# Kernel tuning notes

Measured on AMD Instinct MI355X. Metric: run time of the kernel, lower is better.

The kernel has to match this reference:

```python
import jax, jax.numpy as jnp
import numpy as np

N_NODES = 100000
N_EDGES = 1200000
IN_FEATS = 128
HIDDEN = 64
OUT_FEATS = 40


def setup_inputs() -> dict:
    key = jax.random.key(0)
    k1, k2, k3, k4, k5 = jax.random.split(key, 5)
    x = jax.random.normal(k1, (N_NODES, IN_FEATS), dtype=jnp.float32)
    edge_index = jax.random.randint(k2, (2, N_EDGES), 0, N_NODES, dtype=jnp.int64)
    W1 = jax.random.normal(k3, (IN_FEATS, HIDDEN), dtype=jnp.float32) * (1.0 / np.sqrt(IN_FEATS))
    b1 = jnp.zeros((HIDDEN,), dtype=jnp.float32)
    W2 = jax.random.normal(k4, (HIDDEN, HIDDEN), dtype=jnp.float32) * (1.0 / np.sqrt(HIDDEN))
    b2 = jnp.zeros((HIDDEN,), dtype=jnp.float32)
    Wc = jax.random.normal(k5, (HIDDEN, OUT_FEATS), dtype=jnp.float32) * (1.0 / np.sqrt(HIDDEN))
    bc = jnp.zeros((OUT_FEATS,), dtype=jnp.float32)
    return {"x": x, "edge_index": edge_index, "W1": W1, "b1": b1,
            "W2": W2, "b2": b2, "Wc": Wc, "bc": bc}


def _gcn_norm(edge_index, n_nodes):
    # add self-loops, then symmetric normalization deg^{-1/2}[src] * deg^{-1/2}[dst]
    loops = jnp.arange(n_nodes, dtype=edge_index.dtype)
    src = jnp.concatenate([edge_index[0], loops])
    dst = jnp.concatenate([edge_index[1], loops])
    ones = jnp.ones(src.shape[0], dtype=jnp.float32)
    deg = jax.ops.segment_sum(ones, dst, num_segments=n_nodes)  # in-degree incl. self-loop
    dinv = jnp.where(deg > 0, jax.lax.rsqrt(deg), 0.0)
    norm = dinv[src] * dinv[dst]  # [E+N]
    return src, dst, norm


def _gcn_conv(h, W, b, src, dst, norm, n_nodes):
    h = h @ W                          # [N, F_out] dense transform first (PyG GCNConv)
    msg = h[src] * norm[:, None]       # gather + normalize, [E+N, F_out]
    out = jax.ops.segment_sum(msg, dst, num_segments=n_nodes)  # scatter-add
    return out + b


def reference(x, edge_index, W1, b1, W2, b2, Wc, bc):
    n = x.shape[0]
    src, dst, norm = _gcn_norm(edge_index, n)
    # dropout is identity in eval mode
    h = jax.nn.relu(_gcn_conv(x, W1, b1, src, dst, norm, n))
    embedding = _gcn_conv(h, W2, b2, src, dst, norm, n)
    logits = embedding @ Wc + bc
    soft_label = jax.nn.softmax(logits, axis=1)
    hard_label = jnp.argmax(soft_label, axis=1)
    return (logits, embedding, soft_label, hard_label)
```

## Files before the change

### kernel.cpp

```cpp
#include <hip/hip_runtime.h>
#include <hip/hip_bf16.h>
#include <math.h>

typedef __hip_bfloat16 bf16;

__device__ __forceinline__ float loadf(const void* p, size_t i, bool f32m) {
    return f32m ? ((const float*)p)[i]
                : __bfloat162float(((const bf16*)p)[i]);
}
__device__ __forceinline__ void storef(void* p, size_t i, float v, bool f32m) {
    if (f32m) ((float*)p)[i] = v;
    else      ((bf16*)p)[i] = __float2bfloat16(v);
}
__device__ __forceinline__ int ldidx(const int* w, size_t e, bool e64, size_t E, int row) {
    return e64 ? w[2 * (row * E + e)] : w[row * E + e];
}

__global__ void k_detect(const void* x, const int* ei, float* flags) {
    int lane = threadIdx.x;
    const unsigned short* hx = (const unsigned short*)x;
    unsigned short u = hx[2 * lane];
    int ex = (u >> 7) & 0xFF;
    bool tame = (ex >= 117 && ex <= 136);
    unsigned long long mt = __ballot(tame);
    unsigned long long mz = __ballot(ei[2 * lane + 1] != 0);
    if (lane == 0) {
        flags[0] = (__popcll(mt) >= 48) ? 0.0f : 1.0f;
        flags[1] = (mz == 0ULL) ? 1.0f : 0.0f;
    }
}


__global__ void k_zero_small(int* __restrict__ p, int m) {
    int i = blockIdx.x * 256 + threadIdx.x;
    if (i < m) p[i] = 0;
}

#define SCB_EPT 16

__global__ __launch_bounds__(256) void k_bucket_hist(const int* __restrict__ ei,
                                                     const float* __restrict__ flags,
                                                     int* __restrict__ bcnt, int E, int NB) {
    __shared__ int lcnt[512];
    bool e64 = flags[1] > 0.5f;
    int tid = threadIdx.x;
    for (int i = tid; i < NB; i += 256) lcnt[i] = 0;
    __syncthreads();
    int base = blockIdx.x * 256 * SCB_EPT;
#pragma unroll
    for (int j = 0; j < SCB_EPT; ++j) {
        int e = base + j * 256 + tid;
        if (e < E) atomicAdd(&lcnt[ldidx(ei, e, e64, E, 1) >> 8], 1);
    }
    __syncthreads();
    for (int i = tid; i < NB; i += 256) {
        int c = lcnt[i];
        if (c) atomicAdd(&bcnt[i], c);
    }
}

__global__ __launch_bounds__(512) void k_scan_buckets(const int* __restrict__ bcnt,
                                                      int* __restrict__ bbase,
                                                      int* __restrict__ bcur, int NB) {
    __shared__ int sh[512];
    int tid = threadIdx.x;
    int v = (tid < NB) ? bcnt[tid] : 0;
    sh[tid] = v;
    __syncthreads();
    for (int off = 1; off < 512; off <<= 1) {
        int t = (tid >= off) ? sh[tid - off] : 0;
        __syncthreads();
        sh[tid] += t;
        __syncthreads();
    }
    if (tid < NB) {
        int ex = sh[tid] - v;
        bbase[tid] = ex;
        bcur[tid] = ex;
    }
    if (tid == 0) bbase[NB] = sh[511];
}

__global__ __launch_bounds__(256) void k_bucket_scatter(const int* __restrict__ ei,
                                                        const float* __restrict__ flags,
                                                        int* __restrict__ bcur,
                                                        int2* __restrict__ recs,
                                                        int E, int NB) {
    __shared__ int lcnt[512], lrank[512], lbase[512];
    bool e64 = flags[1] > 0.5f;
    int tid = threadIdx.x;
    for (int i = tid; i < NB; i += 256) { lcnt[i] = 0; lrank[i] = 0; }
    __syncthreads();
    int base = blockIdx.x * 256 * SCB_EPT;
    int s[SCB_EPT], d[SCB_EPT];
#pragma unroll
    for (int j = 0; j < SCB_EPT; ++j) {
        int e = base + j * 256 + tid;
        if (e < E) {
            s[j] = ldidx(ei, e, e64, E, 0);
            d[j] = ldidx(ei, e, e64, E, 1);
            atomicAdd(&lcnt[d[j] >> 8], 1);
        } else d[j] = -1;
    }
    __syncthreads();
    for (int i = tid; i < NB; i += 256) {
        int c = lcnt[i];
        lbase[i] = c ? atomicAdd(&bcur[i], c) : 0;
    }
    __syncthreads();
#pragma unroll
    for (int j = 0; j < SCB_EPT; ++j) {
        if (d[j] >= 0) {
            int b = d[j] >> 8;
            int r = atomicAdd(&lrank[b], 1);
            recs[lbase[b] + r] = make_int2(s[j], d[j]);
        }
    }
}

__global__ __launch_bounds__(256) void k_bucket_csr(const int2* __restrict__ recs,
                                                    const int* __restrict__ bbase,
                                                    int* __restrict__ rowptr,
                                                    float* __restrict__ dinv,
                                                    int* __restrict__ srcs,
                                                    int n, int E) {
    __shared__ int lcnt[256];
    __shared__ int lcur[256];
    int b = blockIdx.x, tid = threadIdx.x;
    int e0 = bbase[b], e1 = bbase[b + 1];
    lcnt[tid] = 0;
    __syncthreads();
    for (int i = e0 + tid; i < e1; i += 256)
        atomicAdd(&lcnt[recs[i].y & 255], 1);
    __syncthreads();
    int c = lcnt[tid];
    lcur[tid] = c;
    __syncthreads();
    for (int off = 1; off < 256; off <<= 1) {
        int t = (tid >= off) ? lcur[tid - off] : 0;
        __syncthreads();
        lcur[tid] += t;
        __syncthreads();
    }
    int rp = bbase[b] + lcur[tid] - c;
    int node = (b << 8) + tid;
    if (node < n) {
        rowptr[node] = rp;
        dinv[node] = rsqrtf((float)(c + 1));
    }
    lcur[tid] = rp;
    __syncthreads();
    for (int i = e0 + tid; i < e1; i += 256) {
        int2 r = recs[i];
        int pos = atomicAdd(&lcur[r.y & 255], 1);
        srcs[pos] = r.x;
    }
    if (b == 0 && tid == 0) rowptr[n] = E;
}

template <int K, bool XF32>
__global__ __launch_bounds__(256) void k_gemm3(const void* __restrict__ Xa,
                                               const void* __restrict__ Xb,
                                               const void* __restrict__ W,
                                               const float* __restrict__ flags,
                                               const float* __restrict__ rowscale,
                                               float* __restrict__ out, int n) {
    __shared__ float xs[64 * (K + 4)];
    __shared__ float wl[K * 68];
    bool f32m = flags[0] > 0.5f;
    const void* X = f32m ? Xa : Xb;
    bool xf32 = XF32 || f32m;
    int tid = threadIdx.x;
    int r0 = blockIdx.x * 64;

    if (f32m) {
        for (int i = tid * 4; i < K * 64; i += 1024) {
            int k = i >> 6, cc = i & 63;
            float4 v = *(const float4*)((const float*)W + i);
            *(float4*)&wl[k * 68 + cc] = v;
        }
    } else {
        for (int i = tid; i < K * 64; i += 256) {
            int k = i >> 6, cc = i & 63;
            wl[k * 68 + cc] = __bfloat162float(((const bf16*)W)[i]);
        }
    }
    if (xf32) {
        for (int i = tid * 4; i < 64 * K; i += 1024) {
            int row = i / K, k = i % K;
            float4 v = {0, 0, 0, 0};
            if (r0 + row < n) v = *(const float4*)((const float*)X + (size_t)(r0 + row) * K + k);
            *(float4*)&xs[row * (K + 4) + k] = v;
        }
    } else {
        for (int i = tid * 4; i < 64 * K; i += 1024) {
            int row = i / K, k = i % K;
            float4 v = {0, 0, 0, 0};
            if (r0 + row < n) {
                const bf16* p = (const bf16*)X + (size_t)(r0 + row) * K + k;
                v.x = __bfloat162float(p[0]); v.y = __bfloat162float(p[1]);
                v.z = __bfloat162float(p[2]); v.w = __bfloat162float(p[3]);
            }
            *(float4*)&xs[row * (K + 4) + k] = v;
        }
    }
    __syncthreads();

    int lane = tid & 63, wv = tid >> 6;
    int rg = lane >> 4, cg = lane & 15;
    int rbase = wv * 16 + rg * 4;
    int cbase = cg * 4;

    float acc[4][4];
#pragma unroll
    for (int r = 0; r < 4; ++r)
#pragma unroll
        for (int c = 0; c < 4; ++c) acc[r][c] = 0.0f;

#pragma unroll 2
    for (int k = 0; k < K; k += 4) {
        float4 xrv[4], wv4[4];
#pragma unroll
        for (int r = 0; r < 4; ++r)
            xrv[r] = *(const float4*)&xs[(rbase + r) * (K + 4) + k];
#pragma unroll
        for (int j = 0; j < 4; ++j)
            wv4[j] = *(const float4*)&wl[(k + j) * 68 + cbase];
#pragma unroll
        for (int r = 0; r < 4; ++r) {
            const float* xp = (const float*)&xrv[r];
#pragma unroll
            for (int j = 0; j < 4; ++j) {
                float xv = xp[j];
                acc[r][0] += xv * wv4[j].x;
                acc[r][1] += xv * wv4[j].y;
                acc[r][2] += xv * wv4[j].z;
                acc[r][3] += xv * wv4[j].w;
            }
        }
    }

#pragma unroll
    for (int r = 0; r < 4; ++r) {
        int row = r0 + rbase + r;
        if (row < n) {
            float sc = rowscale[row];
            float4 st = {acc[r][0] * sc, acc[r][1] * sc, acc[r][2] * sc, acc[r][3] * sc};
            *(float4*)&out[(size_t)row * 64 + cbase] = st;
        }
    }
}

template <int EP>
__global__ __launch_bounds__(256) void k_agg(const float* __restrict__ t,
                                             const float* __restrict__ dinv,
                                             const int* __restrict__ rowptr,
                                             const int* __restrict__ srcs,
                                             const void* __restrict__ bias,
                                             const float* __restrict__ flags,
                                             void* __restrict__ d_out, size_t emb_base,
                                             float* __restrict__ B_ws, int n) {
    bool f32m = flags[0] > 0.5f;
    int wvid = (blockIdx.x * 256 + threadIdx.x) >> 6;
    int lane = threadIdx.x & 63;
    int grp = lane >> 4;
    int col4 = lane & 15;
    int v0 = wvid * 2;
    int v1 = v0 + 1;
    if (v0 >= n) return;
    bool has1 = (v1 < n);

    float4 bias4;
    if (f32m) {
        bias4 = ((const float4*)bias)[col4];
    } else {
        const bf16* bp = (const bf16*)bias + col4 * 4;
        bias4.x = __bfloat162float(bp[0]); bias4.y = __bfloat162float(bp[1]);
        bias4.z = __bfloat162float(bp[2]); bias4.w = __bfloat162float(bp[3]);
    }

    float dvA = dinv[v0];
    float dvB = has1 ? dinv[v1] : 0.0f;
    int e0a = rowptr[v0], e1a = rowptr[v0 + 1];
    int e0b = has1 ? rowptr[v1] : 0;
    int e1b = has1 ? rowptr[v1 + 1] : 0;
    int degA = e1a - e0a + 1;
    int degB = has1 ? (e1b - e0b + 1) : 0;
    int degMax = degA > degB ? degA : degB;

    float4 accA = {0, 0, 0, 0}, accB = {0, 0, 0, 0};

    for (int base = 0; base < degMax; base += 64) {
        int jA = base + lane;
        int sA_l = -1;
        if (jA == 0) sA_l = v0;
        else if (jA < degA) sA_l = srcs[e0a + jA - 1];
        int sB_l = -1;
        if (has1) {
            int jB = base + lane;
            if (jB == 0) sB_l = v1;
            else if (jB < degB) sB_l = srcs[e0b + jB - 1];
        }
        int rem = degMax - base;
        int mq = rem < 64 ? rem : 64;

        for (int q = 0; q < mq; q += 16) {
            int sa[4], sb[4];
#pragma unroll
            for (int u = 0; u < 4; ++u) {
                int idx = q + 4 * u + grp;
                sa[u] = __shfl(sA_l, idx, 64);
                sb[u] = __shfl(sB_l, idx, 64);
            }
            float4 va[4], vb[4];
#pragma unroll
            for (int u = 0; u < 4; ++u) {
                va[u] = make_float4(0, 0, 0, 0);
                if (sa[u] >= 0)
                    va[u] = *((const float4*)(t + ((size_t)sa[u] << 6)) + col4);
                vb[u] = make_float4(0, 0, 0, 0);
                if (sb[u] >= 0)
                    vb[u] = *((const float4*)(t + ((size_t)sb[u] << 6)) + col4);
            }
#pragma unroll
            for (int u = 0; u < 4; ++u) {
                accA.x += va[u].x; accA.y += va[u].y; accA.z += va[u].z; accA.w += va[u].w;
                accB.x += vb[u].x; accB.y += vb[u].y; accB.z += vb[u].z; accB.w += vb[u].w;
            }
        }
    }

#pragma unroll
    for (int off = 16; off < 64; off <<= 1) {
        accA.x += __shfl_xor(accA.x, off, 64);
        accA.y += __shfl_xor(accA.y, off, 64);
        accA.z += __shfl_xor(accA.z, off, 64);
        accA.w += __shfl_xor(accA.w, off, 64);
        accB.x += __shfl_xor(accB.x, off, 64);
        accB.y += __shfl_xor(accB.y, off, 64);
        accB.z += __shfl_xor(accB.z, off, 64);
        accB.w += __shfl_xor(accB.w, off, 64);
    }

    int v = -1; float4 acc; float dv = 0.0f;
    if (grp == 0) { v = v0; acc = accA; dv = dvA; }
    else if (grp == 1 && has1) { v = v1; acc = accB; dv = dvB; }
    if (v >= 0) {
        acc.x = acc.x * dv + bias4.x;
        acc.y = acc.y * dv + bias4.y;
        acc.z = acc.z * dv + bias4.z;
        acc.w = acc.w * dv + bias4.w;
        if (EP == 0) {
            acc.x = fmaxf(acc.x, 0.0f); acc.y = fmaxf(acc.y, 0.0f);
            acc.z = fmaxf(acc.z, 0.0f); acc.w = fmaxf(acc.w, 0.0f);
        }
        size_t ob = (size_t)v * 64 + col4 * 4;
        if (f32m) {
            *(float4*)((float*)d_out + emb_base + ob) = acc;
        } else {
            *(float4*)&B_ws[ob] = acc;
            if (EP == 1) {
                __hip_bfloat162 h0, h1;
                h0.x = __float2bfloat16(acc.x); h0.y = __float2bfloat16(acc.y);
                h1.x = __float2bfloat16(acc.z); h1.y = __float2bfloat16(acc.w);
                __hip_bfloat162* p = (__hip_bfloat162*)((bf16*)d_out + emb_base + ob);
                p[0] = h0; p[1] = h1;
            }
        }
    }
}


__device__ __forceinline__ void store_row40(void* out, size_t base, const float* a, bool f32m) {
    if (f32m) {
        float4* p = (float4*)((float*)out + base);
#pragma unroll
        for (int q = 0; q < 10; ++q) {
            float4 st = {a[q * 4 + 0], a[q * 4 + 1], a[q * 4 + 2], a[q * 4 + 3]};
            p[q] = st;
        }
    } else {
        __hip_bfloat162* p = (__hip_bfloat162*)((bf16*)out + base);
#pragma unroll
        for (int i = 0; i < 20; ++i) {
            __hip_bfloat162 h;
            h.x = __float2bfloat16(a[2 * i]);
            h.y = __float2bfloat16(a[2 * i + 1]);
            p[i] = h;
        }
    }
}

__global__ __launch_bounds__(256) void k_classifier(const float* __restrict__ flags,
                                                    const void* __restrict__ Wc,
                                                    const void* __restrict__ bc,
                                                    void* __restrict__ out,
                                                    size_t emb_base, size_t soft_base,
                                                    size_t hard_base,
                                                    const float* __restrict__ B_ws,
                                                    int n) {
    __shared__ __align__(16) float wcs[64 * 40];
    __shared__ __align__(16) float bcs[40];
    bool f32m = flags[0] > 0.5f;
    const float* emb = f32m ? ((const float*)out + emb_base) : B_ws;
    int tid = threadIdx.x;

    if (f32m) {
        for (int i = tid * 4; i < 64 * 40; i += 1024)
            *(float4*)&wcs[i] = *(const float4*)((const float*)Wc + i);
    } else {
        for (int i = tid; i < 64 * 40; i += 256)
            wcs[i] = __bfloat162float(((const bf16*)Wc)[i]);
    }
    if (tid < 40) bcs[tid] = loadf(bc, tid, f32m);
    __syncthreads();

    int node = blockIdx.x * 256 + tid;
    if (node >= n) return;

    float acc[40];
#pragma unroll
    for (int q = 0; q < 10; ++q) {
        float4 b4 = *(const float4*)&bcs[q * 4];
        acc[q * 4 + 0] = b4.x; acc[q * 4 + 1] = b4.y;
        acc[q * 4 + 2] = b4.z; acc[q * 4 + 3] = b4.w;
    }

    const float4* erow = (const float4*)(emb + (size_t)node * 64);
#pragma unroll 2
    for (int j = 0; j < 16; ++j) {
        float4 e4 = erow[j];
        float ev[4] = {e4.x, e4.y, e4.z, e4.w};
#pragma unroll
        for (int kk = 0; kk < 4; ++kk) {
            float e = ev[kk];
            const float4* wr = (const float4*)&wcs[(j * 4 + kk) * 40];
#pragma unroll
            for (int q = 0; q < 10; ++q) {
                float4 w = wr[q];
                acc[q * 4 + 0] = fmaf(e, w.x, acc[q * 4 + 0]);
                acc[q * 4 + 1] = fmaf(e, w.y, acc[q * 4 + 1]);
                acc[q * 4 + 2] = fmaf(e, w.z, acc[q * 4 + 2]);
                acc[q * 4 + 3] = fmaf(e, w.w, acc[q * 4 + 3]);
            }
        }
    }

    store_row40(out, (size_t)node * 40, acc, f32m);

    float m0 = acc[0], m1 = acc[1], m2 = acc[2], m3 = acc[3];
#pragma unroll
    for (int q = 1; q < 10; ++q) {
        m0 = fmaxf(m0, acc[q * 4 + 0]); m1 = fmaxf(m1, acc[q * 4 + 1]);
        m2 = fmaxf(m2, acc[q * 4 + 2]); m3 = fmaxf(m3, acc[q * 4 + 3]);
    }
    float m = fmaxf(fmaxf(m0, m1), fmaxf(m2, m3));

    int bi = 63;
#pragma unroll
    for (int c = 0; c < 40; ++c)
        if (acc[c] == m && c < bi) bi = c;

    float s = 0.0f;
#pragma unroll
    for (int c = 0; c < 40; ++c) {
        float e = expf(acc[c] - m);
        acc[c] = e;
        s += e;
    }
    float rs = 1.0f / s;
#pragma unroll
    for (int c = 0; c < 40; ++c) acc[c] *= rs;

    store_row40(out, soft_base + (size_t)node * 40, acc, f32m);
    storef(out, hard_base + node, (float)bi, f32m);
}

extern "C" void kernel_launch(void* const* d_in, const int* in_sizes, int n_in,
                              void* d_out, int out_size, void* d_ws, size_t ws_size,
                              hipStream_t stream) {
    const void* x  = d_in[0];
    const int*  ei = (const int*)d_in[1];
    const void* W1 = d_in[2];
    const void* b1 = d_in[3];
    const void* W2 = d_in[4];
    const void* b2 = d_in[5];
    const void* Wc = d_in[6];
    const void* bc = d_in[7];

    const int n = in_sizes[0] / 128;
    const int E = in_sizes[1] / 2;
    const int NB = (n + 255) / 256;

    float* ws    = (float*)d_ws;
    const size_t npad = (((size_t)n + 1023) / 1024) * 1024;
    const size_t Epad = (((size_t)E + 255) / 256) * 256;
    float* flags  = ws;
    int*   bcnt   = (int*)(ws + 256);
    int*   bbase  = (int*)(ws + 768);
    int*   bcur   = (int*)(ws + 1536);
    int*   rowptr = (int*)(ws + 2048);
    float* dinv   = (float*)(rowptr + npad);
    int*   srcs   = (int*)(dinv + npad);
    float* A      = (float*)(srcs + Epad);
    float* B_ws   = A + (size_t)n * 64;
    int2*  recs   = (int2*)B_ws;

    const size_t emb_base  = (size_t)n * 40;
    const size_t soft_base = (size_t)n * 104;
    const size_t hard_base = (size_t)n * 144;
    float* h1_f32m = (float*)d_out + emb_base;

    const int gS  = (E + 256 * SCB_EPT - 1) / (256 * SCB_EPT);
    const int gG  = (n + 63) / 64;
    const int gW  = (n + 7) / 8;
    const int gC  = (n + 255) / 256;

    k_detect<<<1, 64, 0, stream>>>(x, ei, flags);

    k_zero_small<<<2, 256, 0, stream>>>(bcnt, 512);
    k_bucket_hist<<<gS, 256, 0, stream>>>(ei, flags, bcnt, E, NB);
    k_scan_buckets<<<1, 512, 0, stream>>>(bcnt, bbase, bcur, NB);
    k_bucket_scatter<<<gS, 256, 0, stream>>>(ei, flags, bcur, recs, E, NB);
    k_bucket_csr<<<NB, 256, 0, stream>>>(recs, bbase, rowptr, dinv, srcs, n, E);

    k_gemm3<128, false><<<gG, 256, 0, stream>>>(x, x, W1, flags, dinv, A, n);
    k_agg<0><<<gW, 256, 0, stream>>>(A, dinv, rowptr, srcs, b1, flags,
                                     d_out, emb_base, B_ws, n);

    k_gemm3<64, true><<<gG, 256, 0, stream>>>(h1_f32m, B_ws, W2, flags, dinv, A, n);
    k_agg<1><<<gW, 256, 0, stream>>>(A, dinv, rowptr, srcs, b2, flags,
                                     d_out, emb_base, B_ws, n);

    k_classifier<<<gC, 256, 0, stream>>>(flags, Wc, bc, d_out,
                                         emb_base, soft_base, hard_base, B_ws, n);
}
```

Before: 326.5 us.

## Replace FP32 SIMT feature GEMMs with split-bf16 MFMA kernels

The two dense transforms (X@W1 and H@W2) move from a shared-memory FP32 FMA tile kernel to MFMA 16x16x32 bf16 instructions. FP32 inputs are split into hi/lo bf16 parts and three MFMAs per tile recover near-FP32 accuracy. X is now loaded straight from global memory into registers, with no shared-memory staging, and the weights are transposed into shared memory. This cuts the FMA compute cost, at the price of three MFMAs per step, per-element conversion work, and 4-byte scalar output stores in place of float4 stores.

```diff
diff --git a/kernel.cpp b/kernel.cpp
--- a/kernel.cpp
+++ b/kernel.cpp
@@ -3,6 +3,8 @@
 #include <math.h>
 
 typedef __hip_bfloat16 bf16;
+typedef __attribute__((ext_vector_type(8))) short bf16x8;
+typedef __attribute__((ext_vector_type(4))) float f32x4;
 
 __device__ __forceinline__ float loadf(const void* p, size_t i, bool f32m) {
     return f32m ? ((const float*)p)[i]
@@ -14,6 +16,15 @@
 }
 __device__ __forceinline__ int ldidx(const int* w, size_t e, bool e64, size_t E, int row) {
     return e64 ? w[2 * (row * E + e)] : w[row * E + e];
+}
+
+__device__ __forceinline__ unsigned short f2bf(float f) {
+    unsigned u = __float_as_uint(f);
+    unsigned r = (u + 0x7FFFu + ((u >> 16) & 1u)) >> 16;
+    return (unsigned short)r;
+}
+__device__ __forceinline__ float bf2f(unsigned short h) {
+    return __uint_as_float(((unsigned)h) << 16);
 }
 
 __global__ void k_detect(const void* x, const int* ei, float* flags) {
@@ -158,95 +169,99 @@
     if (b == 0 && tid == 0) rowptr[n] = E;
 }
 
-template <int K, bool XF32>
-__global__ __launch_bounds__(256) void k_gemm3(const void* __restrict__ Xa,
-                                               const void* __restrict__ Xb,
-                                               const void* __restrict__ W,
-                                               const float* __restrict__ flags,
-                                               const float* __restrict__ rowscale,
-                                               float* __restrict__ out, int n) {
-    __shared__ float xs[64 * (K + 4)];
-    __shared__ float wl[K * 68];
+template <int K, bool XALWAYSF32>
+__global__ __launch_bounds__(256) void k_gconv_mfma(const void* __restrict__ Xa,
+                                                    const void* __restrict__ Xb,
+                                                    const void* __restrict__ W,
+                                                    const float* __restrict__ flags,
+                                                    const float* __restrict__ rowscale,
+                                                    float* __restrict__ out, int n) {
+    constexpr int KP = K + 8;
+    __shared__ __align__(16) unsigned short wh[64 * KP];
+    __shared__ __align__(16) unsigned short wlo[64 * KP];
     bool f32m = flags[0] > 0.5f;
     const void* X = f32m ? Xa : Xb;
-    bool xf32 = XF32 || f32m;
+    bool xf32 = XALWAYSF32 || f32m;
     int tid = threadIdx.x;
-    int r0 = blockIdx.x * 64;
 
     if (f32m) {
         for (int i = tid * 4; i < K * 64; i += 1024) {
-            int k = i >> 6, cc = i & 63;
+            int k = i >> 6, c = i & 63;
             float4 v = *(const float4*)((const float*)W + i);
-            *(float4*)&wl[k * 68 + cc] = v;
+            float vv[4] = {v.x, v.y, v.z, v.w};
+#pragma unroll
+            for (int q = 0; q < 4; ++q) {
+                unsigned short h = f2bf(vv[q]);
+                unsigned short l = f2bf(vv[q] - bf2f(h));
+                wh [(c + q) * KP + k] = h;
+                wlo[(c + q) * KP + k] = l;
+            }
         }
     } else {
         for (int i = tid; i < K * 64; i += 256) {
-            int k = i >> 6, cc = i & 63;
-            wl[k * 68 + cc] = __bfloat162float(((const bf16*)W)[i]);
-        }
-    }
-    if (xf32) {
-        for (int i = tid * 4; i < 64 * K; i += 1024) {
-            int row = i / K, k = i % K;
-            float4 v = {0, 0, 0, 0};
-            if (r0 + row < n) v = *(const float4*)((const float*)X + (size_t)(r0 + row) * K + k);
-            *(float4*)&xs[row * (K + 4) + k] = v;
-        }
-    } else {
-        for (int i = tid * 4; i < 64 * K; i += 1024) {
-            int row = i / K, k = i % K;
-            float4 v = {0, 0, 0, 0};
-            if (r0 + row < n) {
-                const bf16* p = (const bf16*)X + (size_t)(r0 + row) * K + k;
-                v.x = __bfloat162float(p[0]); v.y = __bfloat162float(p[1]);
-                v.z = __bfloat162float(p[2]); v.w = __bfloat162float(p[3]);
-            }
-            *(float4*)&xs[row * (K + 4) + k] = v;
+            int k = i >> 6, c = i & 63;
+            wh [c * KP + k] = ((const unsigned short*)W)[i];
+            wlo[c * KP + k] = 0;
         }
     }
     __syncthreads();
 
     int lane = tid & 63, wv = tid >> 6;
-    int rg = lane >> 4, cg = lane & 15;
-    int rbase = wv * 16 + rg * 4;
-    int cbase = cg * 4;
-
-    float acc[4][4];
+    int r0 = blockIdx.x * 64 + wv * 16;
+    int mrow = lane & 15, kgrp = lane >> 4;
+    int row = r0 + mrow;
+    bool rok = (row < n);
+
+    f32x4 acc[4];
+#pragma unroll
+    for (int ct = 0; ct < 4; ++ct) acc[ct] = (f32x4){0.0f, 0.0f, 0.0f, 0.0f};
+
+    const float*          xrf = (const float*)X          + (size_t)(rok ? row : 0) * K;
+    const unsigned short* xrb = (const unsigned short*)X + (size_t)(rok ? row : 0) * K;
+
+#pragma unroll
+    for (int ks = 0; ks < K / 32; ++ks) {
+        int kb = ks * 32 + kgrp * 8;
+        bf16x8 ahi = {0, 0, 0, 0, 0, 0, 0, 0};
+        bf16x8 alo = {0, 0, 0, 0, 0, 0, 0, 0};
+        if (rok) {
+            if (xf32) {
+                float4 v0 = *(const float4*)(xrf + kb);
+                float4 v1 = *(const float4*)(xrf + kb + 4);
+                float fv[8] = {v0.x, v0.y, v0.z, v0.w, v1.x, v1.y, v1.z, v1.w};
+#pragma unroll
+                for (int j = 0; j < 8; ++j) {
+                    unsigned short h = f2bf(fv[j]);
+                    ahi[j] = (short)h;
+                    alo[j] = (short)f2bf(fv[j] - bf2f(h));
+                }
+            } else {
+                ahi = *(const bf16x8*)(xrb + kb);
+            }
+        }
+#pragma unroll
+        for (int ct = 0; ct < 4; ++ct) {
+            int c = ct * 16 + mrow;
+            bf16x8 bhi = *(const bf16x8*)&wh [c * KP + kb];
+            bf16x8 blo = *(const bf16x8*)&wlo[c * KP + kb];
+            acc[ct] = __builtin_amdgcn_mfma_f32_16x16x32_bf16(ahi, bhi, acc[ct], 0, 0, 0);
+            acc[ct] = __builtin_amdgcn_mfma_f32_16x16x32_bf16(ahi, blo, acc[ct], 0, 0, 0);
+            acc[ct] = __builtin_amdgcn_mfma_f32_16x16x32_bf16(alo, bhi, acc[ct], 0, 0, 0);
+        }
+    }
+
+    float sc[4];
+    int obase = r0 + kgrp * 4;
 #pragma unroll
     for (int r = 0; r < 4; ++r)
-#pragma unroll
-        for (int c = 0; c < 4; ++c) acc[r][c] = 0.0f;
-
-#pragma unroll 2
-    for (int k = 0; k < K; k += 4) {
-        float4 xrv[4], wv4[4];
-#pragma unroll
-        for (int r = 0; r < 4; ++r)
-            xrv[r] = *(const float4*)&xs[(rbase + r) * (K + 4) + k];
-#pragma unroll
-        for (int j = 0; j < 4; ++j)
-            wv4[j] = *(const float4*)&wl[(k + j) * 68 + cbase];
+        sc[r] = (obase + r < n) ? rowscale[obase + r] : 0.0f;
+#pragma unroll
+    for (int ct = 0; ct < 4; ++ct) {
 #pragma unroll
         for (int r = 0; r < 4; ++r) {
-            const float* xp = (const float*)&xrv[r];
-#pragma unroll
-            for (int j = 0; j < 4; ++j) {
-                float xv = xp[j];
-                acc[r][0] += xv * wv4[j].x;
-                acc[r][1] += xv * wv4[j].y;
-                acc[r][2] += xv * wv4[j].z;
-                acc[r][3] += xv * wv4[j].w;
-            }
-        }
-    }
-
-#pragma unroll
-    for (int r = 0; r < 4; ++r) {
-        int row = r0 + rbase + r;
-        if (row < n) {
-            float sc = rowscale[row];
-            float4 st = {acc[r][0] * sc, acc[r][1] * sc, acc[r][2] * sc, acc[r][3] * sc};
-            *(float4*)&out[(size_t)row * 64 + cbase] = st;
+            int orow = obase + r;
+            if (orow < n)
+                out[(size_t)orow * 64 + ct * 16 + mrow] = acc[ct][r] * sc[r];
         }
     }
 }
@@ -524,11 +539,11 @@
     k_bucket_scatter<<<gS, 256, 0, stream>>>(ei, flags, bcur, recs, E, NB);
     k_bucket_csr<<<NB, 256, 0, stream>>>(recs, bbase, rowptr, dinv, srcs, n, E);
 
-    k_gemm3<128, false><<<gG, 256, 0, stream>>>(x, x, W1, flags, dinv, A, n);
+    k_gconv_mfma<128, false><<<gG, 256, 0, stream>>>(x, x, W1, flags, dinv, A, n);
     k_agg<0><<<gW, 256, 0, stream>>>(A, dinv, rowptr, srcs, b1, flags,
                                      d_out, emb_base, B_ws, n);
 
-    k_gemm3<64, true><<<gG, 256, 0, stream>>>(h1_f32m, B_ws, W2, flags, dinv, A, n);
+    k_gconv_mfma<64, true><<<gG, 256, 0, stream>>>(h1_f32m, B_ws, W2, flags, dinv, A, n);
     k_agg<1><<<gW, 256, 0, stream>>>(A, dinv, rowptr, srcs, b2, flags,
                                      d_out, emb_base, B_ws, n);
 
```

After: 313.1 us. 4.1% less time.
